# Kernel tuning notes

Measured on AMD Instinct MI355X. Metric: run time of the kernel, lower is better.

## Reference

```python
import jax, jax.numpy as jnp
import numpy as np

# --- Mamba2Simple hyperparams (derived from init_kwargs) ---
D_MODEL = 2048
D_STATE = 128
HEADDIM = 64
EXPAND = 2
D_CONV = 4
NGROUPS = 1
CHUNK = 256
EPS = 1e-5
D_INNER = EXPAND * D_MODEL            # 4096
NHEADS = D_INNER // HEADDIM           # 64
CONV_DIM = D_INNER + 2 * NGROUPS * D_STATE          # 4352
D_IN_PROJ = 2 * D_INNER + 2 * NGROUPS * D_STATE + NHEADS  # 8512


def setup_inputs() -> dict:
    key = jax.random.key(0)
    ks = jax.random.split(key, 9)
    B, L = 2, 2048
    x = jax.random.normal(ks[0], (B, L, D_MODEL), jnp.float32)
    w_in = jax.random.normal(ks[1], (D_MODEL, D_IN_PROJ), jnp.float32) * (D_MODEL ** -0.5)
    conv_w = jax.random.normal(ks[2], (CONV_DIM, D_CONV), jnp.float32) * 0.2
    conv_b = jnp.zeros((CONV_DIM,), jnp.float32)
    dt_bias = jax.random.uniform(ks[3], (NHEADS,), jnp.float32, -4.0, -1.0)
    # A in [1, 16] per official init -> A_log = log(A)
    A_log = jnp.log(jax.random.uniform(ks[4], (NHEADS,), jnp.float32, 1.0, 16.0))
    D = jnp.ones((NHEADS,), jnp.float32)
    norm_w = jnp.ones((D_INNER,), jnp.float32)
    w_out = jax.random.normal(ks[5], (D_INNER, D_MODEL), jnp.float32) * (D_INNER ** -0.5)
    return {"x": x, "w_in": w_in, "conv_w": conv_w, "conv_b": conv_b,
            "dt_bias": dt_bias, "A_log": A_log, "D": D, "norm_w": norm_w, "w_out": w_out}


def _segsum(a):
    # a: (..., T) -> (..., T, T) with out[i, j] = sum_{k=j+1..i} a[k] for j<=i else -inf
    T = a.shape[-1]
    cs = jnp.cumsum(a, axis=-1)
    d = cs[..., :, None] - cs[..., None, :]
    mask = jnp.tril(jnp.ones((T, T), dtype=bool))
    return jnp.where(mask, d, -jnp.inf)


def _ssd(X, A, Bm, Cm):
    # X: (b, l, h, p) already multiplied by dt; A: (b, l, h) = dt*A_cont
    # Bm, Cm: (b, l, n)  (ngroups=1, broadcast over heads)
    b, l, h, p = X.shape
    n = Bm.shape[-1]
    c = l // CHUNK
    X = X.reshape(b, c, CHUNK, h, p)
    A = A.reshape(b, c, CHUNK, h).transpose(0, 3, 1, 2)      # (b, h, c, q)
    Bm = Bm.reshape(b, c, CHUNK, n)
    Cm = Cm.reshape(b, c, CHUNK, n)
    A_cs = jnp.cumsum(A, axis=-1)                             # (b, h, c, q)
    Lmat = jnp.exp(_segsum(A))                                # (b, h, c, q, q)
    # intra-chunk (diagonal block) output
    Y_diag = jnp.einsum("bcln,bcsn,bhcls,bcshp->bclhp", Cm, Bm, Lmat, X)
    # per-chunk final states
    decay_states = jnp.exp(A_cs[..., -1:] - A_cs)             # (b, h, c, q)
    states = jnp.einsum("bcln,bhcl,bclhp->bchpn", Bm, decay_states, X)
    # inter-chunk recurrence
    A_last = jnp.pad(A_cs[..., -1], ((0, 0), (0, 0), (1, 0)))  # (b, h, c+1)
    decay_chunk = jnp.exp(_segsum(A_last))                     # (b, h, c+1, c+1)
    states = jnp.concatenate([jnp.zeros_like(states[:, :1]), states], axis=1)
    states = jnp.einsum("bhzc,bchpn->bzhpn", decay_chunk, states)[:, :-1]
    # state -> output contribution
    Y_off = jnp.einsum("bchpn,bcln,bhcl->bclhp", states, Cm, jnp.exp(A_cs))
    return (Y_diag + Y_off).reshape(b, l, h, p)


def _mamba2(x, w_in, conv_w, conv_b, dt_bias, A_log, D, norm_w, w_out):
    B, L, _ = x.shape
    zxbcdt = jnp.einsum("bld,de->ble", x, w_in)               # (B, L, 8512)
    z = zxbcdt[..., :D_INNER]
    xBC = zxbcdt[..., D_INNER:D_INNER + CONV_DIM]
    dt = zxbcdt[..., D_INNER + CONV_DIM:]                      # (B, L, H)
    dt = jax.nn.softplus(dt + dt_bias)
    # causal depthwise conv1d + silu
    xp = jnp.pad(xBC, ((0, 0), (D_CONV - 1, 0), (0, 0)))
    acc = conv_b
    xBC = sum(conv_w[:, k] * xp[:, k:k + L, :] for k in range(D_CONV)) + conv_b
    xBC = jax.nn.silu(xBC)
    xh = xBC[..., :D_INNER].reshape(B, L, NHEADS, HEADDIM)
    Bm = xBC[..., D_INNER:D_INNER + NGROUPS * D_STATE]         # (B, L, N) since ngroups=1
    Cm = xBC[..., D_INNER + NGROUPS * D_STATE:]                # (B, L, N)
    A = -jnp.exp(A_log)                                        # (H,)
    y = _ssd(xh * dt[..., None], dt * A, Bm, Cm)               # (B, L, H, P)
    y = y + xh * D[None, None, :, None]                        # skip term
    y = y.reshape(B, L, D_INNER)
    # gated RMSNorm (norm_before_gate=False): normalize(y * silu(z)) * weight
    y = y * jax.nn.silu(z)
    y = y * jax.lax.rsqrt(jnp.mean(y * y, axis=-1, keepdims=True) + EPS) * norm_w
    return jnp.einsum("ble,ed->bld", y, w_out)


def reference(x, w_in, conv_w, conv_b, dt_bias, A_log, D, norm_w, w_out):
    return x + _mamba2(x, w_in, conv_w, conv_b, dt_bias, A_log, D, norm_w, w_out)
```

## Files before the change

kernel.cpp:

```cpp
#include <hip/hip_runtime.h>
#include <math.h>

#define DEV __device__ __forceinline__

typedef __attribute__((ext_vector_type(4))) float f32x4;
typedef __attribute__((ext_vector_type(4))) unsigned short u16x4;
typedef __attribute__((ext_vector_type(8))) unsigned short u16x8;
typedef __attribute__((ext_vector_type(8))) __bf16 bfv8;

DEV unsigned short f2bf(float f) {
  unsigned u = __builtin_bit_cast(unsigned, f);
  u = (u + 0x7FFFu + ((u >> 16) & 1u)) >> 16;
  return (unsigned short)u;
}
DEV float bf2f(unsigned short h) {
  unsigned u = ((unsigned)h) << 16;
  return __builtin_bit_cast(float, u);
}

DEV f32x4 mfma16(u16x8 a, u16x8 b, f32x4 c) {
  return __builtin_amdgcn_mfma_f32_16x16x32_bf16(
      __builtin_bit_cast(bfv8, a), __builtin_bit_cast(bfv8, b), c, 0, 0, 0);
}

DEV void gload_lds16(const unsigned short* g, unsigned short* s) {
  __builtin_amdgcn_global_load_lds(
      (const __attribute__((address_space(1))) void*)g,
      (__attribute__((address_space(3))) void*)s, 16, 0, 0);
}

template <int N>
DEV void vmcnt_wait() {
  if constexpr (N == 0) asm volatile("s_waitcnt vmcnt(0)" ::: "memory");
  else if constexpr (N == 4) asm volatile("s_waitcnt vmcnt(4)" ::: "memory");
  else if constexpr (N == 8) asm volatile("s_waitcnt vmcnt(8)" ::: "memory");
}

template <int MODE>
__global__ __launch_bounds__(256, 3) void gemm_p(
    const unsigned short* __restrict__ A, const unsigned short* __restrict__ Bt,
    int K, unsigned short* __restrict__ o_z, unsigned short* __restrict__ o_xbc,
    float* __restrict__ o_dt, float* __restrict__ o_c,
    const float* __restrict__ resid) {
  __shared__ __align__(16) unsigned short As[3][128 * 32];
  __shared__ __align__(16) unsigned short Bs[3][128 * 32];
  const int tid = threadIdx.x;
  const int lane = tid & 63, w = tid >> 6;
  const int l16 = lane & 15, lq = lane >> 4;
  const int wr = w >> 1, wc = w & 1;
  const int nwg = gridDim.x * gridDim.y;
  int lin = blockIdx.y * gridDim.x + blockIdx.x;
  lin = (lin & 7) * (nwg >> 3) + (lin >> 3);
  const int m0 = (lin / gridDim.x) * 128, n0 = (lin % gridDim.x) * 128;
  const int lrow = lane >> 2;
  const int gq = (lane & 3) ^ ((lrow >> 1) & 3);
  const int cq = lq ^ ((l16 >> 1) & 3);

  const unsigned short* Ag = A + (size_t)(m0 + lrow) * K + gq * 8;
  const unsigned short* Bg = Bt + (size_t)(n0 + lrow) * K + gq * 8;

  f32x4 acc[4][4] = {};

  auto stage = [&](int bi, int kt) {
#pragma unroll
    for (int i = 0; i < 2; ++i) {
      const int rb = (w + i * 4) * 16;
      gload_lds16(Ag + (size_t)rb * K + kt * 32, &As[bi][rb * 32]);
    }
#pragma unroll
    for (int i = 0; i < 2; ++i) {
      const int rb = (w + i * 4) * 16;
      gload_lds16(Bg + (size_t)rb * K + kt * 32, &Bs[bi][rb * 32]);
    }
  };

  const int nt = K / 32;
  stage(0, 0);
  stage(1, 1);

  for (int k = 0; k < nt; ++k) {
    const int cb = k % 3;
    if (k < nt - 1) vmcnt_wait<4>();
    else vmcnt_wait<0>();
    __builtin_amdgcn_s_barrier();
    if (k + 2 < nt) stage((k + 2) % 3, k + 2);

    u16x8 af[4], bf[4];
#pragma unroll
    for (int mf = 0; mf < 4; ++mf)
      af[mf] = *(const u16x8*)(&As[cb][(wr * 64 + mf * 16 + l16) * 32 + cq * 8]);
#pragma unroll
    for (int nf = 0; nf < 4; ++nf)
      bf[nf] = *(const u16x8*)(&Bs[cb][(wc * 64 + nf * 16 + l16) * 32 + cq * 8]);

    __builtin_amdgcn_s_setprio(1);
#pragma unroll
    for (int mf = 0; mf < 4; ++mf)
#pragma unroll
      for (int nf = 0; nf < 4; ++nf)
        acc[mf][nf] = mfma16(af[mf], bf[nf], acc[mf][nf]);
    __builtin_amdgcn_s_setprio(0);
  }

#pragma unroll
  for (int mf = 0; mf < 4; ++mf) {
#pragma unroll
    for (int nf = 0; nf < 4; ++nf) {
      const int col = n0 + wc * 64 + nf * 16 + l16;
#pragma unroll
      for (int r = 0; r < 4; ++r) {
        const int row = m0 + wr * 64 + mf * 16 + lq * 4 + r;
        float v = acc[mf][nf][r];
        if constexpr (MODE == 0) {
          if (col < 4096) o_z[(size_t)row * 4096 + col] = f2bf(v);
          else if (col < 8448) o_xbc[(size_t)row * 4352 + (col - 4096)] = f2bf(v);
          else if (col < 8512) o_dt[(size_t)row * 64 + (col - 8448)] = v;
        } else {
          size_t idx = (size_t)row * 2048 + col;
          o_c[idx] = v + resid[idx];
        }
      }
    }
  }
}

__global__ __launch_bounds__(256) void convert_bf16(
    const float* __restrict__ in, unsigned short* __restrict__ out) {
  const size_t i = ((size_t)blockIdx.x * 256 + threadIdx.x) * 8;
  f32x4 a = *(const f32x4*)(in + i);
  f32x4 b = *(const f32x4*)(in + i + 4);
  u16x8 o;
#pragma unroll
  for (int j = 0; j < 4; ++j) { o[j] = f2bf(a[j]); o[j + 4] = f2bf(b[j]); }
  *(u16x8*)(out + i) = o;
}

__global__ __launch_bounds__(256) void transpose_conv(
    const float* __restrict__ in, unsigned short* __restrict__ out, int R,
    int C) {
  __shared__ __align__(16) unsigned short T[64][72];
  const int c0 = blockIdx.x * 64, r0 = blockIdx.y * 64;
  const int tid = threadIdx.x;
#pragma unroll
  for (int it = 0; it < 4; ++it) {
    int r = it * 16 + (tid >> 4);
    int c = (tid & 15) * 4;
    f32x4 v = {0.f, 0.f, 0.f, 0.f};
    if (c0 + c < C) v = *(const f32x4*)(in + (size_t)(r0 + r) * C + c0 + c);
#pragma unroll
    for (int j = 0; j < 4; ++j) T[c + j][r] = f2bf(v[j]);
  }
  __syncthreads();
  const int nr = tid >> 2, kc = (tid & 3) * 16;
  u16x8 a = *(const u16x8*)(&T[nr][kc]);
  u16x8 b = *(const u16x8*)(&T[nr][kc + 8]);
  unsigned short* o = out + (size_t)(c0 + nr) * R + r0 + kc;
  *(u16x8*)o = a;
  *(u16x8*)(o + 8) = b;
}

__global__ __launch_bounds__(256) void conv_kernel(
    const unsigned short* __restrict__ raw, const float* __restrict__ cw,
    const float* __restrict__ cb, unsigned short* __restrict__ xbc) {
  const int ch4 = blockIdx.x * 256 + threadIdx.x;
  if (ch4 >= 1088) return;
  const int ch = ch4 * 4;
  const int row = blockIdx.y;
  const int l = row & 2047;
  f32x4 acc = *(const f32x4*)(cb + ch);
  f32x4 w0 = *(const f32x4*)(cw + ch * 4);
  f32x4 w1 = *(const f32x4*)(cw + ch * 4 + 4);
  f32x4 w2 = *(const f32x4*)(cw + ch * 4 + 8);
  f32x4 w3 = *(const f32x4*)(cw + ch * 4 + 12);
#pragma unroll
  for (int k = 0; k < 4; ++k) {
    int ls = l - 3 + k;
    if (ls >= 0) {
      u16x4 v = *(const u16x4*)(raw + (size_t)(row - 3 + k) * 4352 + ch);
      acc[0] += w0[k] * bf2f(v[0]);
      acc[1] += w1[k] * bf2f(v[1]);
      acc[2] += w2[k] * bf2f(v[2]);
      acc[3] += w3[k] * bf2f(v[3]);
    }
  }
  u16x4 o;
#pragma unroll
  for (int j = 0; j < 4; ++j) {
    float s = acc[j] / (1.0f + __expf(-acc[j]));
    o[j] = f2bf(s);
  }
  *(u16x4*)(xbc + (size_t)row * 4352 + ch) = o;
}

__global__ __launch_bounds__(256) void dt_kernel(
    float* __restrict__ dtb, const float* __restrict__ dt_bias,
    const float* __restrict__ A_log, float* __restrict__ Acs) {
  __shared__ float s[256];
  const int blk = blockIdx.x;
  const int c = blk & 7, h = (blk >> 3) & 63, b = blk >> 9;
  const int t = threadIdx.x;
  const int row = b * 2048 + c * 256 + t;
  float xv = dtb[(size_t)row * 64 + h] + dt_bias[h];
  float dt = (xv > 20.0f) ? xv : log1pf(__expf(xv));
  dtb[(size_t)row * 64 + h] = dt;
  float a = dt * (-__expf(A_log[h]));
  s[t] = a;
  __syncthreads();
  for (int off = 1; off < 256; off <<= 1) {
    float v = (t >= off) ? s[t - off] : 0.0f;
    __syncthreads();
    s[t] += v;
    __syncthreads();
  }
  Acs[((size_t)((b * 64 + h) * 8 + c)) * 256 + t] = s[t];
}

__global__ __launch_bounds__(256) void g_kernel(
    const unsigned short* __restrict__ xbc, float* __restrict__ G) {
  const int bc = blockIdx.y;
  const int i0 = (blockIdx.x >> 2) * 64, j0 = (blockIdx.x & 3) * 64;
  const int tid = threadIdx.x;
  const int lane = tid & 63, w = tid >> 6;
  const int l16 = lane & 15, lq = lane >> 4;
  const unsigned short* base = xbc + (size_t)bc * 256 * 4352;
  f32x4 acc[4] = {};
#pragma unroll
  for (int ks = 0; ks < 4; ++ks) {
    int nb = ks * 32 + lq * 8;
    u16x8 af = *(const u16x8*)(base + (size_t)(i0 + w * 16 + l16) * 4352 + 4224 + nb);
#pragma unroll
    for (int jf = 0; jf < 4; ++jf) {
      u16x8 bb = *(const u16x8*)(base + (size_t)(j0 + jf * 16 + l16) * 4352 + 4096 + nb);
      acc[jf] = mfma16(af, bb, acc[jf]);
    }
  }
  float* Gt = G + (size_t)bc * 65536;
#pragma unroll
  for (int jf = 0; jf < 4; ++jf)
#pragma unroll
    for (int r = 0; r < 4; ++r)
      Gt[(i0 + w * 16 + lq * 4 + r) * 256 + j0 + jf * 16 + l16] = acc[jf][r];
}

__global__ __launch_bounds__(512) void ssd_states(
    const unsigned short* __restrict__ xbc, const float* __restrict__ dtb,
    const float* __restrict__ Acs, unsigned short* __restrict__ statesb) {
  __shared__ __align__(16) unsigned short Xt[64 * 264];
  __shared__ __align__(16) unsigned short BmT[128 * 72];
  __shared__ float As_s[256];
  const int h = blockIdx.x, c = blockIdx.y, b = blockIdx.z;
  const int tid = threadIdx.x;
  const int lane = tid & 63, w = tid >> 6;
  const int l16 = lane & 15, lq = lane >> 4;
  const int row0 = b * 2048 + c * 256;

  if (tid < 256) As_s[tid] = Acs[((size_t)((b * 64 + h) * 8 + c)) * 256 + tid];
#pragma unroll
  for (int it = 0; it < 2; ++it) {
    int pb = tid & 15;
    int tb = it * 32 + (tid >> 4);
    float rr[4][4];
#pragma unroll
    for (int i = 0; i < 4; ++i) {
      int row = row0 + tb * 4 + i;
      u16x4 v = *(const u16x4*)(xbc + (size_t)row * 4352 + h * 64 + pb * 4);
      float dtv = dtb[(size_t)row * 64 + h];
#pragma unroll
      for (int j = 0; j < 4; ++j) rr[i][j] = bf2f(v[j]) * dtv;
    }
#pragma unroll
    for (int j = 0; j < 4; ++j) {
      u16x4 hh = {f2bf(rr[0][j]), f2bf(rr[1][j]), f2bf(rr[2][j]), f2bf(rr[3][j])};
      *(u16x4*)(&Xt[(pb * 4 + j) * 264 + tb * 4]) = hh;
    }
  }
  __syncthreads();

  f32x4 accS[4] = {};
  const float Alast = As_s[255];
  for (int part = 0; part < 4; ++part) {
    if (part) __syncthreads();
    {
      int nb = tid & 31;
      int tb = tid >> 5;
      float rr[4][4];
#pragma unroll
      for (int i = 0; i < 4; ++i) {
        int t = part * 64 + tb * 4 + i;
        int row = row0 + t;
        float dec = __expf(Alast - As_s[t]);
        u16x4 v = *(const u16x4*)(xbc + (size_t)row * 4352 + 4096 + nb * 4);
#pragma unroll
        for (int j = 0; j < 4; ++j) rr[i][j] = bf2f(v[j]) * dec;
      }
#pragma unroll
      for (int j = 0; j < 4; ++j) {
        u16x4 hh = {f2bf(rr[0][j]), f2bf(rr[1][j]), f2bf(rr[2][j]), f2bf(rr[3][j])};
        *(u16x4*)(&BmT[(nb * 4 + j) * 72 + tb * 4]) = hh;
      }
    }
    __syncthreads();
#pragma unroll
    for (int ks = 0; ks < 2; ++ks) {
      int toff = ks * 32 + lq * 8;
      u16x8 af = *(const u16x8*)(&BmT[(w * 16 + l16) * 72 + toff]);
#pragma unroll
      for (int pf = 0; pf < 4; ++pf) {
        u16x8 bfr = *(const u16x8*)(&Xt[(pf * 16 + l16) * 264 + part * 64 + toff]);
        accS[pf] = mfma16(af, bfr, accS[pf]);
      }
    }
  }
  unsigned short* Sp = statesb + (size_t)((b * 8 + c) * 64 + h) * 8192;
#pragma unroll
  for (int pf = 0; pf < 4; ++pf) {
    u16x4 hh = {f2bf(accS[pf][0]), f2bf(accS[pf][1]), f2bf(accS[pf][2]),
                f2bf(accS[pf][3])};
    *(u16x4*)(&Sp[(pf * 16 + l16) * 128 + w * 16 + lq * 4]) = hh;
  }
}

__global__ __launch_bounds__(256) void scan_states(
    const unsigned short* __restrict__ statesb, const float* __restrict__ Acs,
    unsigned short* __restrict__ prefix) {
  const int h = blockIdx.x, b = blockIdx.y;
  const int tid = threadIdx.x;
  const int p = tid >> 2, nq = (tid & 3) * 32;
  float S[32];
#pragma unroll
  for (int i = 0; i < 32; ++i) S[i] = 0.0f;
  for (int cc = 0; cc < 8; ++cc) {
    size_t base = (size_t)((b * 8 + cc) * 64 + h) * 8192 + p * 128 + nq;
#pragma unroll
    for (int j = 0; j < 4; ++j) {
      u16x8 hh;
#pragma unroll
      for (int k = 0; k < 8; ++k) hh[k] = f2bf(S[j * 8 + k]);
      *(u16x8*)(prefix + base + j * 8) = hh;
    }
    float eAl = __expf(Acs[((size_t)((b * 64 + h) * 8 + cc)) * 256 + 255]);
#pragma unroll
    for (int j = 0; j < 4; ++j) {
      u16x8 v = *(const u16x8*)(statesb + base + j * 8);
#pragma unroll
      for (int k = 0; k < 8; ++k) S[j * 8 + k] = eAl * S[j * 8 + k] + bf2f(v[k]);
    }
  }
}

__global__ __launch_bounds__(512) void ssd_main(
    const unsigned short* __restrict__ xbc, const float* __restrict__ dtb,
    const float* __restrict__ Acs, const float* __restrict__ G,
    const unsigned short* __restrict__ prefix, const float* __restrict__ Dv,
    unsigned short* __restrict__ y) {
  __shared__ __align__(16) unsigned short Xt[64 * 264];
  __shared__ float As_s[256];
  const int h = blockIdx.x, c = blockIdx.y, b = blockIdx.z;
  const int tid = threadIdx.x;
  const int lane = tid & 63, w = tid >> 6;
  const int l16 = lane & 15, lq = lane >> 4;
  const int row0 = b * 2048 + c * 256;

  if (tid < 256) As_s[tid] = Acs[((size_t)((b * 64 + h) * 8 + c)) * 256 + tid];
#pragma unroll
  for (int it = 0; it < 2; ++it) {
    int pb = tid & 15;
    int tb = it * 32 + (tid >> 4);
    float rr[4][4];
#pragma unroll
    for (int i = 0; i < 4; ++i) {
      int row = row0 + tb * 4 + i;
      u16x4 v = *(const u16x4*)(xbc + (size_t)row * 4352 + h * 64 + pb * 4);
      float dtv = dtb[(size_t)row * 64 + h];
#pragma unroll
      for (int j = 0; j < 4; ++j) rr[i][j] = bf2f(v[j]) * dtv;
    }
#pragma unroll
    for (int j = 0; j < 4; ++j) {
      u16x4 hh = {f2bf(rr[0][j]), f2bf(rr[1][j]), f2bf(rr[2][j]), f2bf(rr[3][j])};
      *(u16x4*)(&Xt[(pb * 4 + j) * 264 + tb * 4]) = hh;
    }
  }
  __syncthreads();

  f32x4 acc[2][4] = {};
  const float* Gt = G + (size_t)(b * 8 + c) * 65536;
  for (int ks = 0; ks < 8; ++ks) {
    const int tb = ks * 32 + lq * 8;
    u16x8 bfr[4];
#pragma unroll
    for (int pf = 0; pf < 4; ++pf)
      bfr[pf] = *(const u16x8*)(&Xt[(pf * 16 + l16) * 264 + tb]);
#pragma unroll
    for (int mf = 0; mf < 2; ++mf) {
      const int i = w * 32 + mf * 16 + l16;
      const float ai = As_s[i];
      const float* gp = Gt + i * 256 + tb;
      f32x4 g0 = *(const f32x4*)gp;
      f32x4 g1 = *(const f32x4*)(gp + 4);
      u16x8 af;
#pragma unroll
      for (int jj = 0; jj < 8; ++jj) {
        int j = tb + jj;
        float g = (jj < 4) ? g0[jj] : g1[jj - 4];
        float v = (i >= j) ? g * __expf(ai - As_s[j]) : 0.0f;
        af[jj] = f2bf(v);
      }
#pragma unroll
      for (int pf = 0; pf < 4; ++pf)
        acc[mf][pf] = mfma16(af, bfr[pf], acc[mf][pf]);
    }
  }
  const unsigned short* Pf = prefix + (size_t)((b * 8 + c) * 64 + h) * 8192;
  for (int ks = 0; ks < 4; ++ks) {
    const int nb = ks * 32 + lq * 8;
    u16x8 bfr[4];
#pragma unroll
    for (int pf = 0; pf < 4; ++pf)
      bfr[pf] = *(const u16x8*)(Pf + (size_t)(pf * 16 + l16) * 128 + nb);
#pragma unroll
    for (int mf = 0; mf < 2; ++mf) {
      const int i = w * 32 + mf * 16 + l16;
      const float eAi = __expf(As_s[i]);
      u16x8 cv = *(const u16x8*)(xbc + (size_t)(row0 + i) * 4352 + 4224 + nb);
      u16x8 af;
#pragma unroll
      for (int jj = 0; jj < 8; ++jj) af[jj] = f2bf(bf2f(cv[jj]) * eAi);
#pragma unroll
      for (int pf = 0; pf < 4; ++pf)
        acc[mf][pf] = mfma16(af, bfr[pf], acc[mf][pf]);
    }
  }
  const float Dh = Dv[h];
#pragma unroll
  for (int mf = 0; mf < 2; ++mf) {
#pragma unroll
    for (int r = 0; r < 4; ++r) {
      int t = w * 32 + mf * 16 + lq * 4 + r;
      size_t row = (size_t)(row0 + t);
#pragma unroll
      for (int pf = 0; pf < 4; ++pf) {
        int p = pf * 16 + l16;
        float xh = bf2f(xbc[row * 4352 + h * 64 + p]);
        y[row * 4096 + h * 64 + p] = f2bf(acc[mf][pf][r] + Dh * xh);
      }
    }
  }
}

__global__ __launch_bounds__(256) void norm_kernel(
    unsigned short* __restrict__ y, const unsigned short* __restrict__ zbf,
    const float* __restrict__ nw) {
  const int row = blockIdx.x, tid = threadIdx.x;
  unsigned short* yr = y + (size_t)row * 4096;
  const unsigned short* zr = zbf + (size_t)row * 4096;
  float vals[16];
  float ss = 0.0f;
#pragma unroll
  for (int i = 0; i < 2; ++i) {
    int cb = i * 2048 + tid * 8;
    u16x8 yv = *(const u16x8*)(yr + cb);
    u16x8 zv = *(const u16x8*)(zr + cb);
#pragma unroll
    for (int j = 0; j < 8; ++j) {
      float z = bf2f(zv[j]);
      float g = bf2f(yv[j]) * (z / (1.0f + __expf(-z)));
      vals[i * 8 + j] = g;
      ss += g * g;
    }
  }
#pragma unroll
  for (int off = 32; off > 0; off >>= 1) ss += __shfl_xor(ss, off, 64);
  __shared__ float red[4];
  if ((tid & 63) == 0) red[tid >> 6] = ss;
  __syncthreads();
  float tot = red[0] + red[1] + red[2] + red[3];
  float rr = rsqrtf(tot * (1.0f / 4096.0f) + 1e-5f);
#pragma unroll
  for (int i = 0; i < 2; ++i) {
    int cb = i * 2048 + tid * 8;
    f32x4 w0 = *(const f32x4*)(nw + cb);
    f32x4 w1 = *(const f32x4*)(nw + cb + 4);
    u16x8 o;
#pragma unroll
    for (int j = 0; j < 8; ++j) {
      float wv = (j < 4) ? w0[j] : w1[j - 4];
      o[j] = f2bf(vals[i * 8 + j] * rr * wv);
    }
    *(u16x8*)(yr + cb) = o;
  }
}

extern "C" void kernel_launch(void* const* d_in, const int* in_sizes, int n_in,
                              void* d_out, int out_size, void* d_ws,
                              size_t ws_size, hipStream_t stream) {
  const float* x = (const float*)d_in[0];
  const float* w_in = (const float*)d_in[1];
  const float* conv_w = (const float*)d_in[2];
  const float* conv_b = (const float*)d_in[3];
  const float* dt_bias = (const float*)d_in[4];
  const float* A_log = (const float*)d_in[5];
  const float* Dvec = (const float*)d_in[6];
  const float* norm_w = (const float*)d_in[7];
  const float* w_out = (const float*)d_in[8];
  float* out = (float*)d_out;

  char* w = (char*)d_ws;
  unsigned short* zbf = (unsigned short*)(w + 0);
  unsigned short* xbc = (unsigned short*)(w + 33554432);
  unsigned short* xbcraw = (unsigned short*)(w + 69206016);
  float* dtb = (float*)(w + 104857600);
  float* Acs = (float*)(w + 105906176);
  float* G = (float*)(w + 106954752);
  unsigned short* statesb = (unsigned short*)(w + 111149056);
  unsigned short* y = (unsigned short*)(w + 127926272);
  unsigned short* xbf = (unsigned short*)(w + 111149056);
  unsigned short* w_inT = (unsigned short*)(w + 33554432);
  unsigned short* w_outT = (unsigned short*)(w + 33554432);
  unsigned short* prefix = xbcraw;

  convert_bf16<<<dim3(4096), 256, 0, stream>>>(x, xbf);
  transpose_conv<<<dim3(136, 32), 256, 0, stream>>>(w_in, w_inT, 2048, 8512);
  gemm_p<0><<<dim3(68, 32), 256, 0, stream>>>(xbf, w_inT, 2048, zbf, xbcraw,
                                              dtb, nullptr, nullptr);
  conv_kernel<<<dim3(5, 4096), 256, 0, stream>>>(xbcraw, conv_w, conv_b, xbc);
  dt_kernel<<<dim3(1024), 256, 0, stream>>>(dtb, dt_bias, A_log, Acs);
  g_kernel<<<dim3(16, 16), 256, 0, stream>>>(xbc, G);
  ssd_states<<<dim3(64, 8, 2), 512, 0, stream>>>(xbc, dtb, Acs, statesb);
  scan_states<<<dim3(64, 2), 256, 0, stream>>>(statesb, Acs, prefix);
  ssd_main<<<dim3(64, 8, 2), 512, 0, stream>>>(xbc, dtb, Acs, G, prefix, Dvec, y);
  transpose_conv<<<dim3(32, 64), 256, 0, stream>>>(w_out, w_outT, 4096, 2048);
  norm_kernel<<<dim3(4096), 256, 0, stream>>>(y, zbf, norm_w);
  gemm_p<1><<<dim3(16, 32), 256, 0, stream>>>(y, w_outT, 4096, nullptr,
                                              nullptr, nullptr, out, x);
}
```

Measured before the change: 496.2 us.

## Add 256x256 eight-wave pipelined GEMM for input projection

Replaces the 128x128 templated GEMM for the input projection with a dedicated 512-thread kernel using 256x256 tiles, K-step 64, double-buffered LDS with XOR swizzle, and global-to-LDS loads interleaved between four MFMA phases. Larger tiles raise arithmetic intensity and reduce LDS/global traffic per MFMA. The output GEMM keeps the old kernel, de-templated. Risks include lower occupancy, a coarser grid with tail imbalance over the CUs, and more barriers per iteration.

```diff
diff --git a/kernel.cpp b/kernel.cpp
--- a/kernel.cpp
+++ b/kernel.cpp
@@ -32,16 +32,142 @@
 template <int N>
 DEV void vmcnt_wait() {
   if constexpr (N == 0) asm volatile("s_waitcnt vmcnt(0)" ::: "memory");
+  else if constexpr (N == 2) asm volatile("s_waitcnt vmcnt(2)" ::: "memory");
   else if constexpr (N == 4) asm volatile("s_waitcnt vmcnt(4)" ::: "memory");
-  else if constexpr (N == 8) asm volatile("s_waitcnt vmcnt(8)" ::: "memory");
-}
-
-template <int MODE>
+}
+
+__global__ __launch_bounds__(512, 2) void gemm8_in(
+    const unsigned short* __restrict__ A, const unsigned short* __restrict__ Bt,
+    unsigned short* __restrict__ o_z, unsigned short* __restrict__ o_xbc,
+    float* __restrict__ o_dt) {
+  constexpr int K = 2048, NT = K / 64;
+  __shared__ __align__(16) unsigned short As[2][256 * 64];
+  __shared__ __align__(16) unsigned short Bs[2][256 * 64];
+  const int tid = threadIdx.x;
+  const int lane = tid & 63, w = tid >> 6;
+  const int l16 = lane & 15, lq = lane >> 4;
+  const int wr = w >> 1, wc = w & 1;
+  const int nwg = gridDim.x * gridDim.y;
+  int lin = blockIdx.y * gridDim.x + blockIdx.x;
+  lin = (lin & 7) * (nwg >> 3) + (lin >> 3);
+  const int m0 = (lin / gridDim.x) * 256, n0 = (lin % gridDim.x) * 256;
+  const int srow = lane >> 3;
+  const int schk = (lane & 7) ^ srow;
+  const unsigned short* Ag = A + (size_t)(m0 + srow) * K + schk * 8;
+  const unsigned short* Bg = Bt + (size_t)(n0 + srow) * K + schk * 8;
+  const int px0 = lq ^ (l16 & 7);
+  const int px1 = (4 + lq) ^ (l16 & 7);
+
+  f32x4 acc[4][8] = {};
+
+  auto stageA = [&](int p, int slot, int kt) {
+    gload_lds16(Ag + (size_t)(slot * 64 + w * 8) * K + kt * 64,
+                &As[p][(slot * 64 + w * 8) * 64]);
+  };
+  auto stageB = [&](int p, int slot, int kt) {
+    gload_lds16(Bg + (size_t)(slot * 64 + w * 8) * K + kt * 64,
+                &Bs[p][(slot * 64 + w * 8) * 64]);
+  };
+  auto rdA = [&](int p, int mf, int k2) -> u16x8 {
+    const int row = wr * 64 + mf * 16 + l16;
+    return *(const u16x8*)(&As[p][row * 64 + (k2 ? px1 : px0) * 8]);
+  };
+  auto rdB = [&](int p, int nf, int k2) -> u16x8 {
+    const int row = wc * 128 + nf * 16 + l16;
+    return *(const u16x8*)(&Bs[p][row * 64 + (k2 ? px1 : px0) * 8]);
+  };
+
+  stageA(0, 0, 0); stageA(0, 1, 0); stageA(0, 2, 0); stageA(0, 3, 0);
+  stageB(0, 0, 0); stageB(0, 2, 0); stageB(0, 1, 0); stageB(0, 3, 0);
+  vmcnt_wait<2>();
+  __builtin_amdgcn_s_barrier();
+
+  u16x8 a0[4], a1[4], b0[2], b1[2];
+  for (int k = 0; k < NT; ++k) {
+    const int p = k & 1, pn = p ^ 1;
+    const bool st = (k + 1 < NT);
+#pragma unroll
+    for (int mf = 0; mf < 4; ++mf) { a0[mf] = rdA(p, mf, 0); a1[mf] = rdA(p, mf, 1); }
+    b0[0] = rdB(p, 0, 0); b1[0] = rdB(p, 0, 1);
+    b0[1] = rdB(p, 1, 0); b1[1] = rdB(p, 1, 1);
+    if (st) { stageA(pn, 0, k + 1); stageA(pn, 1, k + 1); }
+    __builtin_amdgcn_s_barrier();
+    __builtin_amdgcn_s_setprio(1);
+#pragma unroll
+    for (int nf = 0; nf < 2; ++nf)
+#pragma unroll
+      for (int mf = 0; mf < 4; ++mf) {
+        acc[mf][nf] = mfma16(a0[mf], b0[nf], acc[mf][nf]);
+        acc[mf][nf] = mfma16(a1[mf], b1[nf], acc[mf][nf]);
+      }
+    __builtin_amdgcn_s_setprio(0);
+    __builtin_amdgcn_s_barrier();
+    b0[0] = rdB(p, 2, 0); b1[0] = rdB(p, 2, 1);
+    b0[1] = rdB(p, 3, 0); b1[1] = rdB(p, 3, 1);
+    if (st) { stageA(pn, 2, k + 1); stageA(pn, 3, k + 1); vmcnt_wait<4>(); }
+    else vmcnt_wait<0>();
+    __builtin_amdgcn_s_barrier();
+    __builtin_amdgcn_s_setprio(1);
+#pragma unroll
+    for (int nf = 0; nf < 2; ++nf)
+#pragma unroll
+      for (int mf = 0; mf < 4; ++mf) {
+        acc[mf][2 + nf] = mfma16(a0[mf], b0[nf], acc[mf][2 + nf]);
+        acc[mf][2 + nf] = mfma16(a1[mf], b1[nf], acc[mf][2 + nf]);
+      }
+    __builtin_amdgcn_s_setprio(0);
+    __builtin_amdgcn_s_barrier();
+    b0[0] = rdB(p, 4, 0); b1[0] = rdB(p, 4, 1);
+    b0[1] = rdB(p, 5, 0); b1[1] = rdB(p, 5, 1);
+    if (st) { stageB(pn, 0, k + 1); stageB(pn, 2, k + 1); }
+    __builtin_amdgcn_s_barrier();
+    __builtin_amdgcn_s_setprio(1);
+#pragma unroll
+    for (int nf = 0; nf < 2; ++nf)
+#pragma unroll
+      for (int mf = 0; mf < 4; ++mf) {
+        acc[mf][4 + nf] = mfma16(a0[mf], b0[nf], acc[mf][4 + nf]);
+        acc[mf][4 + nf] = mfma16(a1[mf], b1[nf], acc[mf][4 + nf]);
+      }
+    __builtin_amdgcn_s_setprio(0);
+    __builtin_amdgcn_s_barrier();
+    b0[0] = rdB(p, 6, 0); b1[0] = rdB(p, 6, 1);
+    b0[1] = rdB(p, 7, 0); b1[1] = rdB(p, 7, 1);
+    if (st) { stageB(pn, 1, k + 1); stageB(pn, 3, k + 1); vmcnt_wait<2>(); }
+    else vmcnt_wait<0>();
+    __builtin_amdgcn_s_barrier();
+    __builtin_amdgcn_s_setprio(1);
+#pragma unroll
+    for (int nf = 0; nf < 2; ++nf)
+#pragma unroll
+      for (int mf = 0; mf < 4; ++mf) {
+        acc[mf][6 + nf] = mfma16(a0[mf], b0[nf], acc[mf][6 + nf]);
+        acc[mf][6 + nf] = mfma16(a1[mf], b1[nf], acc[mf][6 + nf]);
+      }
+    __builtin_amdgcn_s_setprio(0);
+    __builtin_amdgcn_s_barrier();
+  }
+
+#pragma unroll
+  for (int mf = 0; mf < 4; ++mf) {
+#pragma unroll
+    for (int nf = 0; nf < 8; ++nf) {
+      const int col = n0 + wc * 128 + nf * 16 + l16;
+#pragma unroll
+      for (int r = 0; r < 4; ++r) {
+        const int row = m0 + wr * 64 + mf * 16 + lq * 4 + r;
+        float v = acc[mf][nf][r];
+        if (col < 4096) o_z[(size_t)row * 4096 + col] = f2bf(v);
+        else if (col < 8448) o_xbc[(size_t)row * 4352 + (col - 4096)] = f2bf(v);
+        else if (col < 8512) o_dt[(size_t)row * 64 + (col - 8448)] = v;
+      }
+    }
+  }
+}
+
 __global__ __launch_bounds__(256, 3) void gemm_p(
     const unsigned short* __restrict__ A, const unsigned short* __restrict__ Bt,
-    int K, unsigned short* __restrict__ o_z, unsigned short* __restrict__ o_xbc,
-    float* __restrict__ o_dt, float* __restrict__ o_c,
-    const float* __restrict__ resid) {
+    int K, float* __restrict__ o_c, const float* __restrict__ resid) {
   __shared__ __align__(16) unsigned short As[3][128 * 32];
   __shared__ __align__(16) unsigned short Bs[3][128 * 32];
   const int tid = threadIdx.x;
@@ -110,15 +236,8 @@
 #pragma unroll
       for (int r = 0; r < 4; ++r) {
         const int row = m0 + wr * 64 + mf * 16 + lq * 4 + r;
-        float v = acc[mf][nf][r];
-        if constexpr (MODE == 0) {
-          if (col < 4096) o_z[(size_t)row * 4096 + col] = f2bf(v);
-          else if (col < 8448) o_xbc[(size_t)row * 4352 + (col - 4096)] = f2bf(v);
-          else if (col < 8512) o_dt[(size_t)row * 64 + (col - 8448)] = v;
-        } else {
-          size_t idx = (size_t)row * 2048 + col;
-          o_c[idx] = v + resid[idx];
-        }
+        size_t idx = (size_t)row * 2048 + col;
+        o_c[idx] = acc[mf][nf][r] + resid[idx];
       }
     }
   }
@@ -521,8 +640,7 @@
 
   convert_bf16<<<dim3(4096), 256, 0, stream>>>(x, xbf);
   transpose_conv<<<dim3(136, 32), 256, 0, stream>>>(w_in, w_inT, 2048, 8512);
-  gemm_p<0><<<dim3(68, 32), 256, 0, stream>>>(xbf, w_inT, 2048, zbf, xbcraw,
-                                              dtb, nullptr, nullptr);
+  gemm8_in<<<dim3(34, 16), 512, 0, stream>>>(xbf, w_inT, zbf, xbcraw, dtb);
   conv_kernel<<<dim3(5, 4096), 256, 0, stream>>>(xbcraw, conv_w, conv_b, xbc);
   dt_kernel<<<dim3(1024), 256, 0, stream>>>(dtb, dt_bias, A_log, Acs);
   g_kernel<<<dim3(16, 16), 256, 0, stream>>>(xbc, G);
@@ -531,6 +649,5 @@
   ssd_main<<<dim3(64, 8, 2), 512, 0, stream>>>(xbc, dtb, Acs, G, prefix, Dvec, y);
   transpose_conv<<<dim3(32, 64), 256, 0, stream>>>(w_out, w_outT, 4096, 2048);
   norm_kernel<<<dim3(4096), 256, 0, stream>>>(y, zbf, norm_w);
-  gemm_p<1><<<dim3(16, 32), 256, 0, stream>>>(y, w_outT, 4096, nullptr,
-                                              nullptr, nullptr, out, x);
-}
+  gemm_p<<<dim3(16, 32), 256, 0, stream>>>(y, w_outT, 4096, out, x);
+}
```

After: 480.8 us. 3.1% less time.

## Use per-wave private LDS tiles for input projection GEMM to drop block barriers

Applied to the files above, without the earlier changes.

Adds a new in-projection GEMM kernel in which each wave loads its own 64-row A and B slices into private double-buffered LDS regions. Waves then synchronise only through vmcnt/lgkmcnt waits instead of workgroup barriers. The aim is to remove barrier stalls between waves of the 128x128 tile. In exchange, each A and B slice is loaded twice per block because waves share rows and columns, which doubles global and L2 traffic. Occupancy also drops to 2 blocks per CU.

```diff
diff --git a/kernel.cpp b/kernel.cpp
--- a/kernel.cpp
+++ b/kernel.cpp
@@ -36,12 +36,94 @@
   else if constexpr (N == 8) asm volatile("s_waitcnt vmcnt(8)" ::: "memory");
 }
 
-template <int MODE>
+__global__ __launch_bounds__(256, 2) void gemm_w(
+    const unsigned short* __restrict__ A, const unsigned short* __restrict__ Bt,
+    int K, unsigned short* __restrict__ o_z, unsigned short* __restrict__ o_xbc,
+    float* __restrict__ o_dt) {
+  __shared__ __align__(16) unsigned short As[4][2][64 * 32];
+  __shared__ __align__(16) unsigned short Bs[4][2][64 * 32];
+  const int tid = threadIdx.x;
+  const int lane = tid & 63, w = tid >> 6;
+  const int l16 = lane & 15, lq = lane >> 4;
+  const int wr = w >> 1, wc = w & 1;
+  const int nwg = gridDim.x * gridDim.y;
+  int lin = blockIdx.y * gridDim.x + blockIdx.x;
+  lin = (lin & 7) * (nwg >> 3) + (lin >> 3);
+  const int m0 = (lin / gridDim.x) * 128, n0 = (lin % gridDim.x) * 128;
+  const int lrow = lane >> 2;
+  const int gq = (lane & 3) ^ ((lrow >> 1) & 3);
+  const int cq = lq ^ ((l16 >> 1) & 3);
+
+  const unsigned short* Agw = A + (size_t)(m0 + wr * 64 + lrow) * K + gq * 8;
+  const unsigned short* Bgw = Bt + (size_t)(n0 + wc * 64 + lrow) * K + gq * 8;
+  unsigned short* Aw = &As[w][0][0];
+  unsigned short* Bw = &Bs[w][0][0];
+
+  f32x4 acc[4][4] = {};
+
+  auto stage = [&](int bi, int kt) {
+#pragma unroll
+    for (int i = 0; i < 4; ++i)
+      gload_lds16(Agw + (size_t)(i * 16) * K + kt * 32,
+                  Aw + bi * 2048 + i * 512);
+#pragma unroll
+    for (int i = 0; i < 4; ++i)
+      gload_lds16(Bgw + (size_t)(i * 16) * K + kt * 32,
+                  Bw + bi * 2048 + i * 512);
+  };
+
+  const int nt = K / 32;
+  stage(0, 0);
+  stage(1, 1);
+
+  for (int k = 0; k < nt; ++k) {
+    const int cb = k & 1;
+    if (k < nt - 1) vmcnt_wait<8>();
+    else vmcnt_wait<0>();
+
+    u16x8 af[4], bf[4];
+#pragma unroll
+    for (int mf = 0; mf < 4; ++mf)
+      af[mf] = *(const u16x8*)(Aw + cb * 2048 + (mf * 16 + l16) * 32 + cq * 8);
+#pragma unroll
+    for (int nf = 0; nf < 4; ++nf)
+      bf[nf] = *(const u16x8*)(Bw + cb * 2048 + (nf * 16 + l16) * 32 + cq * 8);
+
+    __builtin_amdgcn_s_setprio(1);
+#pragma unroll
+    for (int mf = 0; mf < 4; ++mf)
+#pragma unroll
+      for (int nf = 0; nf < 4; ++nf)
+        acc[mf][nf] = mfma16(af[mf], bf[nf], acc[mf][nf]);
+    __builtin_amdgcn_s_setprio(0);
+
+    if (k + 2 < nt) {
+      asm volatile("s_waitcnt lgkmcnt(0)" ::: "memory");
+      __builtin_amdgcn_sched_barrier(0);
+      stage(cb, k + 2);
+    }
+  }
+
+#pragma unroll
+  for (int mf = 0; mf < 4; ++mf) {
+#pragma unroll
+    for (int nf = 0; nf < 4; ++nf) {
+      const int col = n0 + wc * 64 + nf * 16 + l16;
+#pragma unroll
+      for (int r = 0; r < 4; ++r) {
+        const int row = m0 + wr * 64 + mf * 16 + lq * 4 + r;
+        float v = acc[mf][nf][r];
+        if (col < 4096) o_z[(size_t)row * 4096 + col] = f2bf(v);
+        else if (col < 8448) o_xbc[(size_t)row * 4352 + (col - 4096)] = f2bf(v);
+        else if (col < 8512) o_dt[(size_t)row * 64 + (col - 8448)] = v;
+      }
+    }
+  }
+}
+
 __global__ __launch_bounds__(256, 3) void gemm_p(
     const unsigned short* __restrict__ A, const unsigned short* __restrict__ Bt,
-    int K, unsigned short* __restrict__ o_z, unsigned short* __restrict__ o_xbc,
-    float* __restrict__ o_dt, float* __restrict__ o_c,
-    const float* __restrict__ resid) {
+    int K, float* __restrict__ o_c, const float* __restrict__ resid) {
   __shared__ __align__(16) unsigned short As[3][128 * 32];
   __shared__ __align__(16) unsigned short Bs[3][128 * 32];
   const int tid = threadIdx.x;
@@ -110,15 +192,8 @@
 #pragma unroll
       for (int r = 0; r < 4; ++r) {
         const int row = m0 + wr * 64 + mf * 16 + lq * 4 + r;
-        float v = acc[mf][nf][r];
-        if constexpr (MODE == 0) {
-          if (col < 4096) o_z[(size_t)row * 4096 + col] = f2bf(v);
-          else if (col < 8448) o_xbc[(size_t)row * 4352 + (col - 4096)] = f2bf(v);
-          else if (col < 8512) o_dt[(size_t)row * 64 + (col - 8448)] = v;
-        } else {
-          size_t idx = (size_t)row * 2048 + col;
-          o_c[idx] = v + resid[idx];
-        }
+        size_t idx = (size_t)row * 2048 + col;
+        o_c[idx] = acc[mf][nf][r] + resid[idx];
       }
     }
   }
@@ -521,8 +596,7 @@
 
   convert_bf16<<<dim3(4096), 256, 0, stream>>>(x, xbf);
   transpose_conv<<<dim3(136, 32), 256, 0, stream>>>(w_in, w_inT, 2048, 8512);
-  gemm_p<0><<<dim3(68, 32), 256, 0, stream>>>(xbf, w_inT, 2048, zbf, xbcraw,
-                                              dtb, nullptr, nullptr);
+  gemm_w<<<dim3(68, 32), 256, 0, stream>>>(xbf, w_inT, 2048, zbf, xbcraw, dtb);
   conv_kernel<<<dim3(5, 4096), 256, 0, stream>>>(xbcraw, conv_w, conv_b, xbc);
   dt_kernel<<<dim3(1024), 256, 0, stream>>>(dtb, dt_bias, A_log, Acs);
   g_kernel<<<dim3(16, 16), 256, 0, stream>>>(xbc, G);
@@ -531,6 +605,5 @@
   ssd_main<<<dim3(64, 8, 2), 512, 0, stream>>>(xbc, dtb, Acs, G, prefix, Dvec, y);
   transpose_conv<<<dim3(32, 64), 256, 0, stream>>>(w_out, w_outT, 4096, 2048);
   norm_kernel<<<dim3(4096), 256, 0, stream>>>(y, zbf, norm_w);
-  gemm_p<1><<<dim3(16, 32), 256, 0, stream>>>(y, w_outT, 4096, nullptr,
-                                              nullptr, nullptr, out, x);
-}
+  gemm_p<<<dim3(16, 32), 256, 0, stream>>>(y, w_outT, 4096, out, x);
+}
```

New measurement: 592.0 us. 19.3% more time.
